# Performance work log

Measured on AMD Instinct MI355X. Metric: run time of the kernel, lower is better.

Reference implementation:

```python
import jax, jax.numpy as jnp
import numpy as np

N_NODES = 100000
N_RELS = 8
N_EDGES = 150000
D_IN = 128
D_OUT = 128


def setup_inputs() -> dict:
    key = jax.random.key(0)
    k1, k2, k3, k4, k5 = jax.random.split(key, 5)
    scale = 1.0 / np.sqrt(D_IN)
    return {
        "x": jax.random.normal(k1, (N_NODES, D_IN), dtype=jnp.float32),
        "weight": jax.random.normal(k2, (N_RELS, D_IN, D_OUT), dtype=jnp.float32) * scale,
        "self_loop_weight": jax.random.normal(k3, (D_IN, D_OUT), dtype=jnp.float32) * scale,
        "bias": jnp.zeros((D_OUT,), dtype=jnp.float32),
        "src": jax.random.randint(k4, (N_RELS, N_EDGES), 0, N_NODES, dtype=jnp.int64),
        "dst": jax.random.randint(k5, (N_RELS, N_EDGES), 0, N_NODES, dtype=jnp.int64),
    }


def reference(x, weight, self_loop_weight, bias, src, dst):
    # Per-relation GraphConv(norm='right'): for each dst node, mean of incoming
    # src features (sum / in-degree, degree clamped to 1), then matmul W_r.
    # HeteroGraphConv sums relation outputs; then self-loop, bias, relu.
    n = x.shape[0]

    def per_rel(s, d, W):
        msgs = jax.ops.segment_sum(x[s], d, num_segments=n)          # [N, D_IN]
        deg = jax.ops.segment_sum(jnp.ones_like(s, dtype=x.dtype), d,
                                  num_segments=n)                     # [N]
        msgs = msgs / jnp.maximum(deg, 1.0)[:, None]
        return msgs @ W                                               # [N, D_OUT]

    agg = jax.vmap(per_rel)(src, dst, weight).sum(axis=0)             # [N, D_OUT]
    out = agg + x @ self_loop_weight + bias
    return jax.nn.relu(out)
```

## Files before the change

### kernel.cpp

```cpp
#include <hip/hip_runtime.h>
#include <hip/hip_bf16.h>
#include <stdint.h>

#define N_NODES 100000
#define N_RELS  8
#define N_EDGES 150000
#define KCOLS   1152
#define CAP     64

#define EB_BLOCKS   587
#define EDGE_SECT   (EB_BLOCKS * N_RELS)
#define CAST_BLOCKS 6250
#define PREP_BLOCKS 576

typedef short bf16x8 __attribute__((ext_vector_type(8)));
typedef float f32x4  __attribute__((ext_vector_type(4)));
typedef unsigned int u32;

__device__ __forceinline__ unsigned short f2b(float f) {
    union { float f; unsigned u; } v; v.f = f;
    unsigned r = v.u + 0x7FFF + ((v.u >> 16) & 1);
    return (unsigned short)(r >> 16);
}

__device__ __forceinline__ void gld16(const void* g, void* lds_uniform) {
    __builtin_amdgcn_global_load_lds(
        (const __attribute__((address_space(1))) u32*)g,
        (__attribute__((address_space(3))) u32*)lds_uniform,
        16, 0, 0);
}


__global__ __launch_bounds__(256) void fused_pre(
    const float* __restrict__ x, const float* __restrict__ W,
    const float* __restrict__ Wself,
    const int* __restrict__ src, const int* __restrict__ dst,
    unsigned short* __restrict__ xb, unsigned short* __restrict__ BT,
    int* __restrict__ cnt, int* __restrict__ ebuf) {
    int b = blockIdx.x;
    if (b < EDGE_SECT) {
        int r = b / EB_BLOCKS, eb = b - r * EB_BLOCKS;
        int e = eb * 256 + threadIdx.x;
        if (e >= N_EDGES) return;
        int s = src[r * N_EDGES + e];
        int d = dst[r * N_EDGES + e];
        int slot = atomicAdd(&cnt[d], 1);
        if (slot < CAP) ebuf[d * CAP + slot] = (r << 17) | s;
    } else if (b < EDGE_SECT + CAST_BLOCKS) {
        int t = (b - EDGE_SECT) * 256 + threadIdx.x;
        if (t >= N_NODES * 16) return;
        int row = t >> 4, g = t & 15;
        const float4* p = (const float4*)(x + (size_t)row * 128 + g * 8);
        float4 a = p[0], bb = p[1];
        unsigned short o[8] = { f2b(a.x), f2b(a.y), f2b(a.z), f2b(a.w),
                                f2b(bb.x), f2b(bb.y), f2b(bb.z), f2b(bb.w) };
        int g2 = (g & 8) | ((g & 7) ^ (row & 7));
        *(int4*)(xb + (size_t)row * 128 + (g2 << 3)) = *(const int4*)o;
    } else {
        int flat = (b - EDGE_SECT - CAST_BLOCKS) * 256 + threadIdx.x;
        if (flat >= 128 * KCOLS) return;
        int n = flat / KCOLS, k = flat - n * KCOLS;
        float v;
        if (k < 1024) {
            int r = k >> 7, kk = k & 127;
            v = W[(r << 14) + (kk << 7) + n];
        } else {
            v = Wself[((k - 1024) << 7) + n];
        }
        int ks = (k & ~63) | ((k & 63) ^ ((n & 7) << 3));
        BT[(size_t)n * KCOLS + ks] = f2b(v);
    }
}

__global__ __launch_bounds__(256) void agg_x(
    const unsigned short* __restrict__ xb, const int* __restrict__ ebuf,
    const int* __restrict__ cnt, unsigned short* __restrict__ Agg) {
    int d = (blockIdx.x << 2) + (threadIdx.x >> 6);
    if (d >= N_NODES) return;
    d = __builtin_amdgcn_readfirstlane(d);
    int lane = threadIdx.x & 63;

    int k = cnt[d]; if (k > CAP) k = CAP;
    k = __builtin_amdgcn_readfirstlane(k);
    int rec = (lane < k) ? ebuf[d * CAP + lane] : -1;
    int rl = rec >> 17;

    const unsigned int* xw = (const unsigned int*)xb;

    unsigned long long mask[8];
#pragma unroll
    for (int r = 0; r < 8; ++r) mask[r] = __ballot(rl == r);

    unsigned long long below = (lane == 63) ? 0x7FFFFFFFFFFFFFFFull
                                            : ((1ull << lane) - 1);
    int pre = 0;
    unsigned long long mymask = 0;
#pragma unroll
    for (int r = 0; r < 8; ++r) {
        pre += (rl > r) ? (int)__popcll(mask[r]) : 0;
        mymask = (rl == r) ? mask[r] : mymask;
    }
    int pos = (rl >= 0) ? (pre + (int)__popcll(mymask & below)) : lane;
    int srt = __builtin_amdgcn_ds_permute(pos << 2, rec);

    int swu = lane ^ ((d & 7) << 2);
    unsigned int* aggRow = (unsigned int*)(Agg + (size_t)d * 1024);

    auto store_r = [&](int rconst, float ax, float ay, int dg) {
        float inv = 1.0f / (float)(dg < 1 ? 1 : dg);
        unsigned int pk = (unsigned int)f2b(ax * inv)
                        | ((unsigned int)f2b(ay * inv) << 16);
        aggRow[(rconst << 6) + swu] = pk;
    };
    auto flush = [&](int r, float ax, float ay) {
        switch (r) {
            case 0: store_r(0, ax, ay, (int)__popcll(mask[0])); break;
            case 1: store_r(1, ax, ay, (int)__popcll(mask[1])); break;
            case 2: store_r(2, ax, ay, (int)__popcll(mask[2])); break;
            case 3: store_r(3, ax, ay, (int)__popcll(mask[3])); break;
            case 4: store_r(4, ax, ay, (int)__popcll(mask[4])); break;
            case 5: store_r(5, ax, ay, (int)__popcll(mask[5])); break;
            case 6: store_r(6, ax, ay, (int)__popcll(mask[6])); break;
            default: store_r(7, ax, ay, (int)__popcll(mask[7])); break;
        }
    };

    float axc = 0.f, ayc = 0.f;
    int cur = 0;
    if (k > 0) cur = __builtin_amdgcn_readlane(srt, 0) >> 17;

    for (int i = 0; i < k; i += 4) {
        int rc4[4];
#pragma unroll
        for (int j = 0; j < 4; ++j) {
            int ii = i + j; if (ii > k - 1) ii = k - 1;
            rc4[j] = __builtin_amdgcn_readlane(srt, ii);
        }
        unsigned int y4[4];
#pragma unroll
        for (int j = 0; j < 4; ++j) {
            int s = rc4[j] & 0x1FFFF;
            y4[j] = xw[(size_t)s * 64 + (lane ^ ((s & 7) << 2))];
        }
#pragma unroll
        for (int j = 0; j < 4; ++j) {
            if (i + j < k) {
                int rr = rc4[j] >> 17;
                if (rr != cur) {
                    flush(cur, axc, ayc);
                    axc = 0.f; ayc = 0.f; cur = rr;
                }
                union { unsigned u; float f; } vx, vy;
                vx.u = y4[j] << 16;
                vy.u = y4[j] & 0xFFFF0000u;
                axc += vx.f;
                ayc += vy.f;
            }
        }
    }
    if (k > 0) flush(cur, axc, ayc);

#pragma unroll
    for (int r = 0; r < 8; ++r)
        if (mask[r] == 0) aggRow[(r << 6) + swu] = 0u;
}

__global__ __launch_bounds__(256) void gemm_out(
    const unsigned short* __restrict__ Agg, const unsigned short* __restrict__ xb,
    const unsigned short* __restrict__ BT, const float* __restrict__ bias,
    float* __restrict__ out) {
    __shared__ short As[2][128 * 64];
    __shared__ short Bs[2][128 * 64];
    int t = threadIdx.x;
    int rowBase = blockIdx.x * 128;

    int w = t >> 6, lane = t & 63;
    int wr = w >> 1, wc = w & 1;
    int ml = lane & 15, quad = lane >> 4;
    int sa = (lane & 7) << 4;

    int ri = lane >> 3;
    int cb = (lane & 7) << 4;

    f32x4 acc[4][4];
#pragma unroll
    for (int i = 0; i < 4; ++i)
#pragma unroll
        for (int j = 0; j < 4; ++j)
            acc[i][j] = (f32x4){0.f, 0.f, 0.f, 0.f};

    auto stage = [&](int buf, int t2) {
        int kc = t2 >> 1, h = t2 & 1;
#pragma unroll
        for (int j = 0; j < 4; ++j) {
            int i = (w << 2) + j;
            int row = (i << 3) + ri;
            int grow = rowBase + row;
            if (grow > N_NODES - 1) grow = N_NODES - 1;
            const char* ga = (kc < 8)
                ? (const char*)Agg + (size_t)grow * 2048 + (kc << 8) + (h << 7) + cb
                : (const char*)xb  + (size_t)grow * 256  + (h << 7) + cb;
            gld16(ga, (char*)&As[buf][0] + (i << 10));
            const char* gb = (const char*)BT + (size_t)row * 2304 + (t2 << 7) + cb;
            gld16(gb, (char*)&Bs[buf][0] + (i << 10));
        }
    };

    auto compute = [&](int buf) {
#pragma unroll
        for (int kb = 0; kb < 2; ++kb) {
            int off = ((kb << 6) + (quad << 4)) ^ sa;
            bf16x8 a[4], b[4];
#pragma unroll
            for (int i = 0; i < 4; ++i)
                a[i] = *(const bf16x8*)((const char*)&As[buf][0] +
                        (((wr << 6) + (i << 4) + ml) << 7) + off);
#pragma unroll
            for (int j = 0; j < 4; ++j)
                b[j] = *(const bf16x8*)((const char*)&Bs[buf][0] +
                        (((wc << 6) + (j << 4) + ml) << 7) + off);
#pragma unroll
            for (int i = 0; i < 4; ++i)
#pragma unroll
                for (int j = 0; j < 4; ++j)
                    acc[i][j] = __builtin_amdgcn_mfma_f32_16x16x32_bf16(a[i], b[j], acc[i][j], 0, 0, 0);
        }
    };

    stage(0, 0);
    asm volatile("s_waitcnt vmcnt(0)" ::: "memory");
    __syncthreads();
    int cur = 0;
    for (int t2 = 0; t2 < 18; ++t2) {
        if (t2 + 1 < 18) stage(cur ^ 1, t2 + 1);
        compute(cur);
        asm volatile("s_waitcnt vmcnt(0)" ::: "memory");
        __syncthreads();
        cur ^= 1;
    }

#pragma unroll
    for (int i = 0; i < 4; ++i) {
#pragma unroll
        for (int j = 0; j < 4; ++j) {
            int col = wc * 64 + j * 16 + ml;
            float bv = bias[col];
#pragma unroll
            for (int rr = 0; rr < 4; ++rr) {
                int row = rowBase + wr * 64 + i * 16 + quad * 4 + rr;
                if (row < N_NODES) {
                    float v = acc[i][j][rr] + bv;
                    out[(size_t)row * 128 + col] = fmaxf(v, 0.f);
                }
            }
        }
    }
}

extern "C" void kernel_launch(void* const* d_in, const int* in_sizes, int n_in,
                              void* d_out, int out_size, void* d_ws, size_t ws_size,
                              hipStream_t stream) {
    const float* x     = (const float*)d_in[0];
    const float* W     = (const float*)d_in[1];
    const float* Wself = (const float*)d_in[2];
    const float* bias  = (const float*)d_in[3];
    const int*   src   = (const int*)d_in[4];
    const int*   dst   = (const int*)d_in[5];
    float* out = (float*)d_out;

    char* ws = (char*)d_ws;
    size_t off = 0;
    unsigned short* Agg = (unsigned short*)(ws + off); off += (size_t)N_NODES * 1024 * 2;
    unsigned short* xb  = (unsigned short*)(ws + off); off += (size_t)N_NODES * 128 * 2;
    unsigned short* BT  = (unsigned short*)(ws + off); off += (size_t)128 * KCOLS * 2;
    int* cnt  = (int*)(ws + off); off += (size_t)N_NODES * 4;
    int* ebuf = (int*)(ws + off); off += (size_t)N_NODES * CAP * 4;

    hipMemsetAsync(cnt, 0, (size_t)N_NODES * 4, stream);

    fused_pre<<<EDGE_SECT + CAST_BLOCKS + PREP_BLOCKS, 256, 0, stream>>>(
        x, W, Wself, src, dst, xb, BT, cnt, ebuf);

    agg_x<<<(N_NODES + 3) / 4, 256, 0, stream>>>(xb, ebuf, cnt, Agg);

    gemm_out<<<(N_NODES + 127) / 128, 256, 0, stream>>>(Agg, xb, BT, bias, out);
}
```

Before: 329.0 us.

## Batch edge bucketing, deepen gather unroll, and read GEMM B operand directly from global

Edge bucketing now handles four edges per thread in fewer blocks, issuing the loads before the atomics. The aggregation gather loop is unrolled from 4 to 8 edges so more loads are in flight. The GEMM stops staging the weight matrix in LDS: the swizzle is removed from BT and each wave reads its B fragments straight from global memory, which halves shared memory per block, and launch bounds now ask for four blocks per CU. The aim is better occupancy and fewer LDS transfers, at the cost of uncoalesced B fragment reads that depend on cache hits.

After: 375.1 us. 1.14x slower.

```diff
diff --git a/kernel.cpp b/kernel.cpp
--- a/kernel.cpp
+++ b/kernel.cpp
@@ -8,10 +8,11 @@
 #define KCOLS   1152
 #define CAP     64
 
-#define EB_BLOCKS   587
-#define EDGE_SECT   (EB_BLOCKS * N_RELS)
+#define EB_UNITS    147
+#define EDGE_SECT   (EB_UNITS * N_RELS)
 #define CAST_BLOCKS 6250
 #define PREP_BLOCKS 576
+#define TOTAL_PRE   (EDGE_SECT + CAST_BLOCKS + PREP_BLOCKS)
 
 typedef short bf16x8 __attribute__((ext_vector_type(8)));
 typedef float f32x4  __attribute__((ext_vector_type(4)));
@@ -38,37 +39,50 @@
     unsigned short* __restrict__ xb, unsigned short* __restrict__ BT,
     int* __restrict__ cnt, int* __restrict__ ebuf) {
     int b = blockIdx.x;
+    int tid = threadIdx.x;
     if (b < EDGE_SECT) {
-        int r = b / EB_BLOCKS, eb = b - r * EB_BLOCKS;
-        int e = eb * 256 + threadIdx.x;
-        if (e >= N_EDGES) return;
-        int s = src[r * N_EDGES + e];
-        int d = dst[r * N_EDGES + e];
-        int slot = atomicAdd(&cnt[d], 1);
-        if (slot < CAP) ebuf[d * CAP + slot] = (r << 17) | s;
+        int r = b / EB_UNITS, eb = b - r * EB_UNITS;
+        int e0 = eb * 1024 + tid;
+        const int* sp = src + r * N_EDGES;
+        const int* dp = dst + r * N_EDGES;
+        int ss[4], dd[4], slot[4];
+#pragma unroll
+        for (int j = 0; j < 4; ++j) {
+            int e = e0 + j * 256;
+            if (e < N_EDGES) { ss[j] = sp[e]; dd[j] = dp[e]; }
+            else dd[j] = -1;
+        }
+#pragma unroll
+        for (int j = 0; j < 4; ++j)
+            if (dd[j] >= 0) slot[j] = atomicAdd(&cnt[dd[j]], 1);
+#pragma unroll
+        for (int j = 0; j < 4; ++j)
+            if (dd[j] >= 0 && slot[j] < CAP)
+                ebuf[dd[j] * CAP + slot[j]] = (r << 17) | ss[j];
     } else if (b < EDGE_SECT + CAST_BLOCKS) {
-        int t = (b - EDGE_SECT) * 256 + threadIdx.x;
-        if (t >= N_NODES * 16) return;
-        int row = t >> 4, g = t & 15;
-        const float4* p = (const float4*)(x + (size_t)row * 128 + g * 8);
-        float4 a = p[0], bb = p[1];
-        unsigned short o[8] = { f2b(a.x), f2b(a.y), f2b(a.z), f2b(a.w),
-                                f2b(bb.x), f2b(bb.y), f2b(bb.z), f2b(bb.w) };
-        int g2 = (g & 8) | ((g & 7) ^ (row & 7));
-        *(int4*)(xb + (size_t)row * 128 + (g2 << 3)) = *(const int4*)o;
+        int t = (b - EDGE_SECT) * 256 + tid;
+        if (t < N_NODES * 16) {
+            int row = t >> 4, g = t & 15;
+            const float4* p = (const float4*)(x + (size_t)row * 128 + g * 8);
+            float4 a = p[0], bb = p[1];
+            unsigned short o[8] = { f2b(a.x), f2b(a.y), f2b(a.z), f2b(a.w),
+                                    f2b(bb.x), f2b(bb.y), f2b(bb.z), f2b(bb.w) };
+            int g2 = (g & 8) | ((g & 7) ^ (row & 7));
+            *(int4*)(xb + (size_t)row * 128 + (g2 << 3)) = *(const int4*)o;
+        }
     } else {
-        int flat = (b - EDGE_SECT - CAST_BLOCKS) * 256 + threadIdx.x;
-        if (flat >= 128 * KCOLS) return;
-        int n = flat / KCOLS, k = flat - n * KCOLS;
-        float v;
-        if (k < 1024) {
-            int r = k >> 7, kk = k & 127;
-            v = W[(r << 14) + (kk << 7) + n];
-        } else {
-            v = Wself[((k - 1024) << 7) + n];
-        }
-        int ks = (k & ~63) | ((k & 63) ^ ((n & 7) << 3));
-        BT[(size_t)n * KCOLS + ks] = f2b(v);
+        int flat = (b - EDGE_SECT - CAST_BLOCKS) * 256 + tid;
+        if (flat < 128 * KCOLS) {
+            int n = flat / KCOLS, k = flat - n * KCOLS;
+            float v;
+            if (k < 1024) {
+                int r = k >> 7, kk = k & 127;
+                v = W[(r << 14) + (kk << 7) + n];
+            } else {
+                v = Wself[((k - 1024) << 7) + n];
+            }
+            BT[flat] = f2b(v);
+        }
     }
 }
 
@@ -129,30 +143,30 @@
     int cur = 0;
     if (k > 0) cur = __builtin_amdgcn_readlane(srt, 0) >> 17;
 
-    for (int i = 0; i < k; i += 4) {
-        int rc4[4];
-#pragma unroll
-        for (int j = 0; j < 4; ++j) {
+    for (int i = 0; i < k; i += 8) {
+        int rc8[8];
+#pragma unroll
+        for (int j = 0; j < 8; ++j) {
             int ii = i + j; if (ii > k - 1) ii = k - 1;
-            rc4[j] = __builtin_amdgcn_readlane(srt, ii);
-        }
-        unsigned int y4[4];
-#pragma unroll
-        for (int j = 0; j < 4; ++j) {
-            int s = rc4[j] & 0x1FFFF;
-            y4[j] = xw[(size_t)s * 64 + (lane ^ ((s & 7) << 2))];
-        }
-#pragma unroll
-        for (int j = 0; j < 4; ++j) {
+            rc8[j] = __builtin_amdgcn_readlane(srt, ii);
+        }
+        unsigned int y8[8];
+#pragma unroll
+        for (int j = 0; j < 8; ++j) {
+            int s = rc8[j] & 0x1FFFF;
+            y8[j] = xw[(size_t)s * 64 + (lane ^ ((s & 7) << 2))];
+        }
+#pragma unroll
+        for (int j = 0; j < 8; ++j) {
             if (i + j < k) {
-                int rr = rc4[j] >> 17;
+                int rr = rc8[j] >> 17;
                 if (rr != cur) {
                     flush(cur, axc, ayc);
                     axc = 0.f; ayc = 0.f; cur = rr;
                 }
                 union { unsigned u; float f; } vx, vy;
-                vx.u = y4[j] << 16;
-                vy.u = y4[j] & 0xFFFF0000u;
+                vx.u = y8[j] << 16;
+                vy.u = y8[j] & 0xFFFF0000u;
                 axc += vx.f;
                 ayc += vy.f;
             }
@@ -165,12 +179,11 @@
         if (mask[r] == 0) aggRow[(r << 6) + swu] = 0u;
 }
 
-__global__ __launch_bounds__(256) void gemm_out(
+__global__ __launch_bounds__(256, 4) void gemm_out(
     const unsigned short* __restrict__ Agg, const unsigned short* __restrict__ xb,
     const unsigned short* __restrict__ BT, const float* __restrict__ bias,
     float* __restrict__ out) {
     __shared__ short As[2][128 * 64];
-    __shared__ short Bs[2][128 * 64];
     int t = threadIdx.x;
     int rowBase = blockIdx.x * 128;
 
@@ -201,12 +214,10 @@
                 ? (const char*)Agg + (size_t)grow * 2048 + (kc << 8) + (h << 7) + cb
                 : (const char*)xb  + (size_t)grow * 256  + (h << 7) + cb;
             gld16(ga, (char*)&As[buf][0] + (i << 10));
-            const char* gb = (const char*)BT + (size_t)row * 2304 + (t2 << 7) + cb;
-            gld16(gb, (char*)&Bs[buf][0] + (i << 10));
         }
     };
 
-    auto compute = [&](int buf) {
+    auto compute = [&](int buf, int t2) {
 #pragma unroll
         for (int kb = 0; kb < 2; ++kb) {
             int off = ((kb << 6) + (quad << 4)) ^ sa;
@@ -216,9 +227,11 @@
                 a[i] = *(const bf16x8*)((const char*)&As[buf][0] +
                         (((wr << 6) + (i << 4) + ml) << 7) + off);
 #pragma unroll
-            for (int j = 0; j < 4; ++j)
-                b[j] = *(const bf16x8*)((const char*)&Bs[buf][0] +
-                        (((wc << 6) + (j << 4) + ml) << 7) + off);
+            for (int j = 0; j < 4; ++j) {
+                int n = (wc << 6) + (j << 4) + ml;
+                b[j] = *(const bf16x8*)&BT[(size_t)n * KCOLS +
+                        (t2 << 6) + (kb << 5) + (quad << 3)];
+            }
 #pragma unroll
             for (int i = 0; i < 4; ++i)
 #pragma unroll
@@ -233,7 +246,7 @@
     int cur = 0;
     for (int t2 = 0; t2 < 18; ++t2) {
         if (t2 + 1 < 18) stage(cur ^ 1, t2 + 1);
-        compute(cur);
+        compute(cur, t2);
         asm volatile("s_waitcnt vmcnt(0)" ::: "memory");
         __syncthreads();
         cur ^= 1;
@@ -278,8 +291,8 @@
 
     hipMemsetAsync(cnt, 0, (size_t)N_NODES * 4, stream);
 
-    fused_pre<<<EDGE_SECT + CAST_BLOCKS + PREP_BLOCKS, 256, 0, stream>>>(
-        x, W, Wself, src, dst, xb, BT, cnt, ebuf);
+    fused_pre<<<TOTAL_PRE, 256, 0, stream>>>(x, W, Wself, src, dst,
+                                             xb, BT, cnt, ebuf);
 
     agg_x<<<(N_NODES + 3) / 4, 256, 0, stream>>>(xb, ebuf, cnt, Agg);
 
```
